# Kernel tuning notes

Hardware: AMD Instinct MI355X
Metric: run time of the kernel (lower is better)

## Reference

```python
import jax, jax.numpy as jnp
import numpy as np

B_SZ, N, D = 16, 256, 64


def setup_inputs() -> dict:
    key = jax.random.key(0)
    kA, kB, kl1, kl2, kl3 = jax.random.split(key, 5)

    def pair_mask(k):
        # per-graph number of valid nodes in [N//2, N); mask over node pairs
        lengths = jax.random.randint(k, (B_SZ,), N // 2, N)
        valid = jnp.arange(N)[None, :] < lengths[:, None]          # (b, n)
        return valid[:, :, None] & valid[:, None, :]               # (b, n, n)

    A_mask = pair_mask(kl1)
    B_mask = pair_mask(kl2)
    tar_mask = pair_mask(kl3)
    A_data = jax.random.normal(kA, (B_SZ, N, N), dtype=jnp.float32)
    B_data = jax.random.normal(kB, (B_SZ, N, N, D), dtype=jnp.float32)
    return {
        "A_data": A_data,
        "A_mask": A_mask,
        "B_data": B_data,
        "B_mask": B_mask,
        "tar_mask": tar_mask,
    }


def reference(A_data, A_mask, B_data, B_mask, tar_mask):
    # MaskedTensor semantics: zero-fill masked entries before the contraction.
    Af = jnp.where(A_mask, A_data, jnp.zeros((), A_data.dtype))            # (b, i, j)
    Bf = jnp.where(B_mask[..., None], B_data, jnp.zeros((), B_data.dtype))  # (b, j, k, d)
    # mamamm with dim1=2 (A's j), dim2=1 (B's j): bij,bjkd->bikd
    out = jnp.einsum("bij,bjkd->bikd", Af, Bf)
    # Output masked by the target mask.
    return jnp.where(tar_mask[..., None], out, jnp.zeros((), out.dtype))
```

## Files before the change

kernel.cpp:

```cpp
#include <hip/hip_runtime.h>


typedef __attribute__((ext_vector_type(8))) short short8;
typedef __attribute__((ext_vector_type(4))) float f32x4;

static __device__ __forceinline__ unsigned short f2bf(float f){
  union { float f; unsigned u; } v; v.f = f;
  unsigned r = v.u + 0x7FFFu + ((v.u >> 16) & 1u);
  return (unsigned short)(r >> 16);
}

static __device__ __forceinline__ unsigned char mask_elem(const void* p, long i, int flag){
  switch(flag){
    case 0:  return ((const unsigned char*)p)[i] ? 1 : 0;
    case 1:  return ((const int*)p)[i] ? 1 : 0;
    case 2:  return ((const long long*)p)[i] ? 1 : 0;
    case 3:  return ((const float*)p)[i] != 0.f ? 1 : 0;
    default: return ((const double*)p)[i] != 0.0 ? 1 : 0;
  }
}

__global__ void detect_k(const unsigned char* m, int* flag){
  unsigned char b0=m[0], b1=m[1], b3=m[3], b4=m[4];
  int f;
  if(b0==1 && b1==1)      f = 0;
  else if(b0==1)          f = (b4==1)?1:2;
  else                    f = (b3==0x3f)?3:4;
  *flag = f;
}

__global__ __launch_bounds__(256) void prep_A2(const float* __restrict__ A,
    const void* __restrict__ Am, unsigned short* __restrict__ Abf,
    const int* __restrict__ flagp){
  int flag = *flagp;
  long base = ((long)blockIdx.x*256 + threadIdx.x)*8;
  float4 a0 = *(const float4*)(A+base), a1 = *(const float4*)(A+base+4);
  unsigned char m[8];
  if(flag == 0){
    unsigned long long w = *(const unsigned long long*)((const unsigned char*)Am + base);
#pragma unroll
    for(int e=0;e<8;e++) m[e] = (unsigned char)((w >> (e*8)) & 0xffull);
  } else if(flag == 1){
    const int4* p = (const int4*)((const int*)Am + base);
    int4 w0 = p[0], w1 = p[1];
    m[0]=w0.x!=0;m[1]=w0.y!=0;m[2]=w0.z!=0;m[3]=w0.w!=0;
    m[4]=w1.x!=0;m[5]=w1.y!=0;m[6]=w1.z!=0;m[7]=w1.w!=0;
  } else {
#pragma unroll
    for(int e=0;e<8;e++) m[e] = mask_elem(Am, base+e, flag);
  }
  float f[8] = {a0.x,a0.y,a0.z,a0.w,a1.x,a1.y,a1.z,a1.w};
  short8 o;
#pragma unroll
  for(int e=0;e<8;e++) o[e] = (short)f2bf(m[e] ? f[e] : 0.f);
  *(short8*)(Abf+base) = o;
}

__global__ __launch_bounds__(256) void prep_masks2(const void* __restrict__ Bm,
    const void* __restrict__ Tm, unsigned char* __restrict__ BmT,
    unsigned char* __restrict__ tarT, unsigned long long* __restrict__ rowBbits,
    unsigned long long* __restrict__ kvalbits, const int* __restrict__ flagp){
  int flag = *flagp;
  int b = blockIdx.x;
  int tr = blockIdx.y >> 2, tc = blockIdx.y & 3;
  int which = blockIdx.z;
  const void* src = which ? Tm : Bm;
  __shared__ unsigned char tile[64][65];
  long base = (long)b*65536;
  int t = threadIdx.x;
#pragma unroll
  for(int p=0;p<16;p++){
    int rr = p*4 + (t>>6), cc = t&63;
    tile[rr][cc] = mask_elem(src, base + (long)(tr*64+rr)*256 + tc*64+cc, flag);
  }
  __syncthreads();
  unsigned char* dst = which ? tarT : BmT;
#pragma unroll
  for(int p=0;p<16;p++){
    int oc = p*4 + (t>>6), wj = t&63;
    dst[base + (long)(tc*64+oc)*256 + tr*64 + wj] = tile[wj][oc];
  }
  if(t < 64){
    unsigned char o = 0;
    if(which == 0){
#pragma unroll
      for(int cbit=0;cbit<64;cbit++) o |= tile[t][cbit];
      unsigned long long bal = __ballot(o != 0);
      if(t == 0) atomicOr(&rowBbits[b*4 + tr], bal);
    } else {
#pragma unroll
      for(int r=0;r<64;r++) o |= tile[r][t];
      unsigned long long bal = __ballot(o != 0);
      if(t == 0) atomicOr(&kvalbits[b*4 + tc], bal);
    }
  }
}

__global__ __launch_bounds__(256) void mm_k(
    const unsigned short* __restrict__ Abf, const float* __restrict__ B,
    const unsigned char* __restrict__ BmT, const unsigned char* __restrict__ tarT,
    const unsigned long long* __restrict__ kvalbits,
    const unsigned long long* __restrict__ rowBbits,
    float* __restrict__ out)
{
  int bid0 = blockIdx.x;
  int bid = (bid0 & 7)*512 + (bid0 >> 3);
  int b = bid >> 8, k = bid & 255;
  int t = threadIdx.x, lane = t & 63, wave = t >> 6;

  __shared__ int4 Bt[2048];

  f32x4 acc[4][4];
#pragma unroll
  for(int mi=0;mi<4;mi++)
#pragma unroll
    for(int ni=0;ni<4;ni++)
      acc[mi][ni] = (f32x4){0.f,0.f,0.f,0.f};

  int kv = (int)((kvalbits[b*4 + (k>>6)] >> (k & 63)) & 1ull);
  unsigned long long rb0=rowBbits[b*4], rb1=rowBbits[b*4+1],
                     rb2=rowBbits[b*4+2], rb3=rowBbits[b*4+3];

  if(kv){
    int d = lane, jt = wave;
    unsigned long long rbw = jt==0?rb0 : jt==1?rb1 : jt==2?rb2 : rb3;
    if(rbw){
      const float* Bsrc = B + (size_t)b*4194304 + (size_t)k*64 + d;
      const unsigned long long* bm8 =
          (const unsigned long long*)(BmT + ((size_t)bid<<8) + jt*64);
#pragma unroll
      for(int jc=0; jc<8; jc++){
        int j0 = jt*64 + jc*8;
        unsigned long long mw = bm8[jc];
        int pk[4];
#pragma unroll
        for(int e=0; e<4; e++){
          int j = j0 + e*2;
          float f0 = 0.f, f1 = 0.f;
          if((mw >> (e*16)) & 0xffull)     f0 = Bsrc[(size_t)j << 14];
          if((mw >> (e*16+8)) & 0xffull)   f1 = Bsrc[(size_t)(j+1) << 14];
          pk[e] = (int)f2bf(f0) | ((int)f2bf(f1) << 16);
        }
        int byt = (d*512 + j0*2) ^ ((d & 7) << 4);
        Bt[byt >> 4] = make_int4(pk[0], pk[1], pk[2], pk[3]);
      }
    }
  }
  __syncthreads();

  if(kv){
    const unsigned short* Arow = Abf + ((size_t)b << 16) + (size_t)(wave*64 + (lane & 15))*256;
    int qq = lane >> 4;
#pragma unroll
    for(int ks=0; ks<8; ks++){
      unsigned long long rbw = (ks>>1)==0?rb0 : (ks>>1)==1?rb1 : (ks>>1)==2?rb2 : rb3;
      if(!rbw) continue;
      int jcol = ks*32 + qq*8;
      short8 af[4], bfr[4];
#pragma unroll
      for(int mi=0; mi<4; mi++)
        af[mi] = *(const short8*)(Arow + mi*4096 + jcol);
#pragma unroll
      for(int ni=0; ni<4; ni++){
        int dd = ni*16 + (lane & 15);
        int byt = (dd*512 + jcol*2) ^ ((dd & 7) << 4);
        union { int4 i; short8 s; } u; u.i = Bt[byt >> 4];
        bfr[ni] = u.s;
      }
#pragma unroll
      for(int mi=0; mi<4; mi++)
#pragma unroll
        for(int ni=0; ni<4; ni++)
          acc[mi][ni] = __builtin_amdgcn_mfma_f32_16x16x32_bf16(bfr[ni], af[mi], acc[mi][ni], 0, 0, 0);
    }
  }

  const unsigned char* tb = tarT + ((size_t)bid << 8);
  float* ob = out + (size_t)b*4194304 + (size_t)k*64;
  int q = lane >> 4, c = lane & 15;
#pragma unroll
  for(int mi=0; mi<4; mi++){
    int i = wave*64 + mi*16 + c;
    float tm = tb[i] ? 1.f : 0.f;
#pragma unroll
    for(int ni=0; ni<4; ni++){
      f32x4 v = acc[mi][ni];
      float4 w = make_float4(v[0]*tm, v[1]*tm, v[2]*tm, v[3]*tm);
      *(float4*)(ob + (size_t)i*16384 + ni*16 + q*4) = w;
    }
  }
}

extern "C" void kernel_launch(void* const* d_in, const int* in_sizes, int n_in,
                              void* d_out, int out_size, void* d_ws, size_t ws_size,
                              hipStream_t stream) {
  const float* A  = (const float*)d_in[0];
  const void*  Am = d_in[1];
  const float* Bd = (const float*)d_in[2];
  const void*  Bm = d_in[3];
  const void*  Tm = d_in[4];
  float* out = (float*)d_out;

  char* ws = (char*)d_ws;
  unsigned short* Abf  = (unsigned short*)ws;
  unsigned char*  BmT  = (unsigned char*)(ws + (2u<<20));
  unsigned char*  tarT = (unsigned char*)(ws + (3u<<20));
  unsigned long long* rowBbits = (unsigned long long*)(ws + (4u<<20));
  unsigned long long* kvalbits = (unsigned long long*)(ws + (4u<<20) + 512);
  int*            flag = (int*)(ws + (4u<<20) + 1024);

  hipMemsetAsync(ws + (4u<<20), 0, 1024, stream);
  detect_k   <<<1, 1, 0, stream>>>((const unsigned char*)Am, flag);
  prep_A2    <<<512, 256, 0, stream>>>(A, Am, Abf, flag);
  prep_masks2<<<dim3(16,16,2), 256, 0, stream>>>(Bm, Tm, BmT, tarT, rowBbits, kvalbits, flag);
  mm_k       <<<4096, 256, 0, stream>>>(Abf, Bd, BmT, tarT, kvalbits, rowBbits, out);
}
```

Baseline: 507.6 us.

## Double-buffer B staging across j-chunks and overlap loads with MFMA

Splits the j dimension into four 64-wide stages, each staged into one of two smaller LDS buffers, so loading and bf16-packing the next chunk of B overlaps the MFMA work on the current chunk. LDS per block drops from 32KB to 16KB and launch bounds request 3 blocks per CU to raise occupancy. Each stage issues its 16 strided B loads unconditionally and applies the mask afterwards, instead of a load per pair guarded by the mask. This adds more barriers, and the extra live registers may conflict with the occupancy target.

```diff
diff --git a/kernel.cpp b/kernel.cpp
--- a/kernel.cpp
+++ b/kernel.cpp
@@ -96,7 +96,7 @@
   }
 }
 
-__global__ __launch_bounds__(256) void mm_k(
+__global__ __launch_bounds__(256, 3) void mm_k(
     const unsigned short* __restrict__ Abf, const float* __restrict__ B,
     const unsigned char* __restrict__ BmT, const unsigned char* __restrict__ tarT,
     const unsigned long long* __restrict__ kvalbits,
@@ -108,7 +108,7 @@
   int b = bid >> 8, k = bid & 255;
   int t = threadIdx.x, lane = t & 63, wave = t >> 6;
 
-  __shared__ int4 Bt[2048];
+  __shared__ int4 Bt[2][512];
 
   f32x4 acc[4][4];
 #pragma unroll
@@ -118,53 +118,58 @@
       acc[mi][ni] = (f32x4){0.f,0.f,0.f,0.f};
 
   int kv = (int)((kvalbits[b*4 + (k>>6)] >> (k & 63)) & 1ull);
-  unsigned long long rb0=rowBbits[b*4], rb1=rowBbits[b*4+1],
-                     rb2=rowBbits[b*4+2], rb3=rowBbits[b*4+3];
-
-  if(kv){
-    int d = lane, jt = wave;
-    unsigned long long rbw = jt==0?rb0 : jt==1?rb1 : jt==2?rb2 : rb3;
-    if(rbw){
-      const float* Bsrc = B + (size_t)b*4194304 + (size_t)k*64 + d;
-      const unsigned long long* bm8 =
-          (const unsigned long long*)(BmT + ((size_t)bid<<8) + jt*64);
-#pragma unroll
-      for(int jc=0; jc<8; jc++){
-        int j0 = jt*64 + jc*8;
-        unsigned long long mw = bm8[jc];
-        int pk[4];
-#pragma unroll
-        for(int e=0; e<4; e++){
-          int j = j0 + e*2;
-          float f0 = 0.f, f1 = 0.f;
-          if((mw >> (e*16)) & 0xffull)     f0 = Bsrc[(size_t)j << 14];
-          if((mw >> (e*16+8)) & 0xffull)   f1 = Bsrc[(size_t)(j+1) << 14];
-          pk[e] = (int)f2bf(f0) | ((int)f2bf(f1) << 16);
-        }
-        int byt = (d*512 + j0*2) ^ ((d & 7) << 4);
-        Bt[byt >> 4] = make_int4(pk[0], pk[1], pk[2], pk[3]);
+  int rb[4];
+#pragma unroll
+  for(int s=0;s<4;s++) rb[s] = kv && (rowBbits[b*4 + s] != 0ull);
+
+  const float* Bsrc = B + (size_t)b*4194304 + (size_t)k*64 + lane;
+  const unsigned char* bmrow = BmT + ((size_t)bid << 8);
+
+  auto STAGE = [&](int s, int buf){
+    int j0 = s*64 + wave*16;
+    uint4 mw = *(const uint4*)(bmrow + j0);
+    int byt0 = (lane*128 + wave*32) ^ ((lane & 7) << 4);
+    if((mw.x | mw.y | mw.z | mw.w) != 0u){
+      const float* p = Bsrc + (size_t)j0*16384;
+      float f[16];
+#pragma unroll
+      for(int jj=0;jj<16;jj++) f[jj] = p[(size_t)jj*16384];
+      unsigned mb[4] = {mw.x, mw.y, mw.z, mw.w};
+      int pk[8];
+#pragma unroll
+      for(int e=0;e<8;e++){
+        unsigned w = mb[e>>1];
+        unsigned m0 = (w >> ((e&1)*16))     & 0xffu;
+        unsigned m1 = (w >> ((e&1)*16 + 8)) & 0xffu;
+        float f0 = m0 ? f[2*e]   : 0.f;
+        float f1 = m1 ? f[2*e+1] : 0.f;
+        pk[e] = (int)f2bf(f0) | ((int)f2bf(f1) << 16);
       }
-    }
-  }
-  __syncthreads();
-
-  if(kv){
-    const unsigned short* Arow = Abf + ((size_t)b << 16) + (size_t)(wave*64 + (lane & 15))*256;
-    int qq = lane >> 4;
-#pragma unroll
-    for(int ks=0; ks<8; ks++){
-      unsigned long long rbw = (ks>>1)==0?rb0 : (ks>>1)==1?rb1 : (ks>>1)==2?rb2 : rb3;
-      if(!rbw) continue;
-      int jcol = ks*32 + qq*8;
+      Bt[buf][byt0 >> 4]        = make_int4(pk[0],pk[1],pk[2],pk[3]);
+      Bt[buf][(byt0 ^ 16) >> 4] = make_int4(pk[4],pk[5],pk[6],pk[7]);
+    } else {
+      int4 z = make_int4(0,0,0,0);
+      Bt[buf][byt0 >> 4]        = z;
+      Bt[buf][(byt0 ^ 16) >> 4] = z;
+    }
+  };
+
+  auto COMPUTE = [&](int s, int buf){
+    const unsigned short* Arow = Abf + ((size_t)b << 16)
+        + (size_t)(wave*64 + (lane & 15))*256 + s*64;
+    int qq = lane >> 4, c15 = lane & 15;
+#pragma unroll
+    for(int ksub=0; ksub<2; ksub++){
+      int jc = ksub*32 + qq*8;
       short8 af[4], bfr[4];
 #pragma unroll
       for(int mi=0; mi<4; mi++)
-        af[mi] = *(const short8*)(Arow + mi*4096 + jcol);
+        af[mi] = *(const short8*)(Arow + mi*4096 + jc);
 #pragma unroll
       for(int ni=0; ni<4; ni++){
-        int dd = ni*16 + (lane & 15);
-        int byt = (dd*512 + jcol*2) ^ ((dd & 7) << 4);
-        union { int4 i; short8 s; } u; u.i = Bt[byt >> 4];
+        int dd = ni*16 + c15;
+        int byt = (dd*128 + jc*2) ^ ((dd & 7) << 4);
+        union { int4 i; short8 s; } u; u.i = Bt[buf][byt >> 4];
         bfr[ni] = u.s;
       }
 #pragma unroll
@@ -173,6 +178,15 @@
         for(int ni=0; ni<4; ni++)
           acc[mi][ni] = __builtin_amdgcn_mfma_f32_16x16x32_bf16(bfr[ni], af[mi], acc[mi][ni], 0, 0, 0);
     }
+  };
+
+  if(rb[0]) STAGE(0, 0);
+  __syncthreads();
+#pragma unroll
+  for(int s=0; s<4; s++){
+    if(s < 3 && rb[s+1]) STAGE(s+1, (s+1)&1);
+    if(rb[s])            COMPUTE(s, s&1);
+    __syncthreads();
   }
 
   const unsigned char* tb = tarT + ((size_t)bid << 8);
```

New measurement: 488.9 us. 1.04x faster.
